# Kernel optimization log

Hardware: AMD Instinct MI355X
Metric: run time of the kernel (lower is better)

The kernel has to match this reference:

```python
import jax, jax.numpy as jnp
import numpy as np

HIDDEN = 128
AUG = 2          # aug_dim
SUBSTEPS = 2     # fixed dopri5 substeps per output interval (replaces adaptive stepping)
B = 16384
T = 8


def _xavier(key, shape, gain=5.0 / 3.0):
    fan_in, fan_out = shape
    lim = gain * np.sqrt(6.0 / (fan_in + fan_out))
    return jax.random.uniform(key, shape, jnp.float32, -lim, lim)


def setup_inputs() -> dict:
    key = jax.random.key(0)
    ks = jax.random.split(key, 4)
    return {
        "r0": jax.random.normal(ks[0], (B, 2), jnp.float32),
        "t": jnp.linspace(0.0, 1.0, T, dtype=jnp.float32),
        "W1": _xavier(ks[1], (5, HIDDEN)),
        "b1": jnp.zeros((HIDDEN,), jnp.float32),
        "W2": _xavier(ks[2], (HIDDEN, HIDDEN)),
        "b2": jnp.zeros((HIDDEN,), jnp.float32),
        "W3": _xavier(ks[3], (HIDDEN, 2)),
        "b3": jnp.zeros((2,), jnp.float32),
    }


def _ode_f(t, s, W1, b1, W2, b2, W3, b3):
    # s: [B, 2+AUG]; t: scalar -> concat time feature, tiny tanh MLP
    tf = t * jnp.ones((s.shape[0], 1), s.dtype)
    inp = jnp.concatenate([s, tf], axis=-1)            # [B, 5]
    h = jnp.tanh(inp @ W1 + b1)                        # [B, 128]
    h = jnp.tanh(h @ W2 + b2)                          # [B, 128]
    v_xy = h @ W3 + b3                                 # [B, 2]
    v_a = jnp.zeros((s.shape[0], AUG), s.dtype)        # static aug dynamics
    return jnp.concatenate([v_xy, v_a], axis=-1)


def _dopri5_step(f, t, s, dt):
    # Dormand-Prince RK45 tableau, 5th-order solution advance (as torchdiffeq dopri5)
    k1 = f(t, s)
    k2 = f(t + dt * (1.0 / 5.0), s + dt * (1.0 / 5.0) * k1)
    k3 = f(t + dt * (3.0 / 10.0), s + dt * ((3.0 / 40.0) * k1 + (9.0 / 40.0) * k2))
    k4 = f(t + dt * (4.0 / 5.0),
           s + dt * ((44.0 / 45.0) * k1 - (56.0 / 15.0) * k2 + (32.0 / 9.0) * k3))
    k5 = f(t + dt * (8.0 / 9.0),
           s + dt * ((19372.0 / 6561.0) * k1 - (25360.0 / 2187.0) * k2
                     + (64448.0 / 6561.0) * k3 - (212.0 / 729.0) * k4))
    k6 = f(t + dt,
           s + dt * ((9017.0 / 3168.0) * k1 - (355.0 / 33.0) * k2
                     + (46732.0 / 5247.0) * k3 + (49.0 / 176.0) * k4
                     - (5103.0 / 18656.0) * k5))
    return s + dt * ((35.0 / 384.0) * k1 + (500.0 / 1113.0) * k3
                     + (125.0 / 192.0) * k4 - (2187.0 / 6784.0) * k5
                     + (11.0 / 84.0) * k6)


def _integrate(r0, t, W1, b1, W2, b2, W3, b3):
    s0 = jnp.concatenate([r0, jnp.zeros((r0.shape[0], AUG), r0.dtype)], axis=-1)
    f = lambda tt, ss: _ode_f(tt, ss, W1, b1, W2, b2, W3, b3)

    def interval(s, ts):
        t0, t1 = ts
        dt = (t1 - t0) / SUBSTEPS
        for j in range(SUBSTEPS):  # small fixed loop, unrolled
            s = _dopri5_step(f, t0 + j * dt, s, dt)
        return s, s

    _, ys = jax.lax.scan(interval, s0, (t[:-1], t[1:]))   # [T-1, B, 4]
    traj = jnp.concatenate([s0[None], ys], axis=0)        # [T, B, 4]
    return jnp.transpose(traj, (1, 0, 2))[..., :2]        # [B, T, 2]


def reference(r0, t, W1, b1, W2, b2, W3, b3):
    return _integrate(r0, t, W1, b1, W2, b2, W3, b3)
```

## Files before the change

### kernel.cpp

```cpp
#include <hip/hip_runtime.h>


#define HID 128
#define TT  8
#define F(a,b) ((float)((double)(a)/(double)(b)))
#define K2C 2.8853900817779268f

typedef __attribute__((ext_vector_type(8))) short bf16x8;
typedef __attribute__((ext_vector_type(4))) float f32x4;
typedef __attribute__((ext_vector_type(2))) float f32x2;

union Frag { bf16x8 v; unsigned short u[8]; unsigned int d[4]; };

__device__ __forceinline__ f32x2 bc(float s) { return f32x2{s, s}; }
__device__ __forceinline__ f32x2 pk_fma(f32x2 a, f32x2 b, f32x2 c) {
#if __has_builtin(__builtin_elementwise_fma)
  return __builtin_elementwise_fma(a, b, c);
#else
  return a * b + c;
#endif
}
__device__ __forceinline__ float exp2_fast(float x) {
#if __has_builtin(__builtin_amdgcn_exp2f)
  return __builtin_amdgcn_exp2f(x);
#else
  return __builtin_exp2f(x);
#endif
}
__device__ __forceinline__ unsigned short f2bf(float f) {
  unsigned u = __builtin_bit_cast(unsigned, f);
  u += 0x7FFFu + ((u >> 16) & 1u);
  return (unsigned short)(u >> 16);
}
__device__ __forceinline__ unsigned pack2bf(float a, float b) {
#if __has_builtin(__builtin_amdgcn_cvt_pk_bf16_f32)
  auto pk = __builtin_amdgcn_cvt_pk_bf16_f32(a, b);
  return __builtin_bit_cast(unsigned, pk);
#else
  unsigned ua = __builtin_bit_cast(unsigned, a);
  unsigned ub = __builtin_bit_cast(unsigned, b);
  ua += 0x7FFFu + ((ua >> 16) & 1u);
  ub += 0x7FFFu + ((ub >> 16) & 1u);
  return __builtin_amdgcn_perm(ub, ua, 0x07060302u);
#endif
}
__device__ __forceinline__ f32x2 sig_q(f32x2 u) {
  f32x2 e;
  e.x = exp2_fast(u.x);
  e.y = exp2_fast(u.y);
  f32x2 d = e + bc(1.0f);
  f32x2 q;
  q.x = __builtin_amdgcn_rcpf(d.x);
  q.y = __builtin_amdgcn_rcpf(d.y);
  return q;
}
__device__ __forceinline__ f32x2 tanh_pre(f32x2 u) {
  return pk_fma(bc(-2.0f), sig_q(u), bc(1.0f));
}

__global__ __launch_bounds__(64, 1) void node_kernel(
    const float* __restrict__ r0, const float* __restrict__ tarr,
    const float* __restrict__ W1, const float* __restrict__ b1,
    const float* __restrict__ W2, const float* __restrict__ b2,
    const float* __restrict__ W3, const float* __restrict__ b3,
    float* __restrict__ out)
{
  const int lane = (int)(threadIdx.x & 63u);
  const int quad = lane >> 4;
  const int m16  = lane & 15;
  const int s    = (int)blockIdx.x * 16 + m16;

  f32x2 w1x[16], w1y[16], w1t[16], bb1[16];
  #pragma unroll
  for (int kk = 0; kk < 4; ++kk)
    #pragma unroll
    for (int p = 0; p < 4; ++p) {
      int i = kk * 32 + quad * 8 + 2 * p;
      int idx = kk * 4 + p;
      w1x[idx] = f32x2{W1[0 * HID + i], W1[0 * HID + i + 1]} * bc(K2C);
      w1y[idx] = f32x2{W1[1 * HID + i], W1[1 * HID + i + 1]} * bc(K2C);
      w1t[idx] = f32x2{W1[4 * HID + i], W1[4 * HID + i + 1]} * bc(K2C);
      bb1[idx] = f32x2{b1[i], b1[i + 1]} * bc(K2C);
    }
  Frag W2f[8][4];
  #pragma unroll
  for (int t = 0; t < 8; ++t) {
    int o = t * 16 + m16;
    #pragma unroll
    for (int kk = 0; kk < 4; ++kk) {
      #pragma unroll
      for (int j = 0; j < 8; ++j)
        W2f[t][kk].u[j] = f2bf(W2[(kk * 32 + quad * 8 + j) * HID + o] * K2C);
      asm volatile("" : "+a"(W2f[t][kk].v));
    }
  }
  f32x4 b2i[8];
  f32x2 w3n2[8][4];
  f32x2 w3s = bc(0.f);
  #pragma unroll
  for (int t = 0; t < 8; ++t) {
    #pragma unroll
    for (int rr = 0; rr < 4; ++rr) {
      int o = t * 16 + quad * 4 + rr;
      b2i[t][rr] = b2[o] * K2C;
      f32x2 w3 = f32x2{W3[o * 2 + 0], W3[o * 2 + 1]};
      w3s += w3;
      w3n2[t][rr] = w3 * bc(-2.f);
    }
    asm volatile("" : "+a"(b2i[t]));
  }
  const f32x2 b3v = f32x2{b3[0], b3[1]};

  f32x2 S = f32x2{r0[2 * s + 0], r0[2 * s + 1]};
  if (lane < 16) *(float2*)&out[(s * TT + 0) * 2] = make_float2(S.x, S.y);

  auto feval = [&](float tt, f32x2 st) -> f32x2 {
    const f32x2 sx = bc(st.x), sy = bc(st.y), tv = bc(tt);
    f32x4 acc[8];
    #pragma unroll
    for (int kk = 0; kk < 4; ++kk) {
      unsigned pd[4];
      #pragma unroll
      for (int p = 0; p < 4; ++p) {
        int idx = kk * 4 + p;
        f32x2 a = pk_fma(sx, w1x[idx], bb1[idx]);
        a = pk_fma(sy, w1y[idx], a);
        a = pk_fma(tv, w1t[idx], a);
        f32x2 h = tanh_pre(a);
        pd[p] = pack2bf(h.x, h.y);
      }
      Frag bv;
      bv.d[0] = pd[0]; bv.d[1] = pd[1]; bv.d[2] = pd[2]; bv.d[3] = pd[3];
      if (kk == 0) {
        #pragma unroll
        for (int t = 0; t < 8; ++t)
          acc[t] = __builtin_amdgcn_mfma_f32_16x16x32_bf16(
              W2f[t][0].v, bv.v, b2i[t], 0, 0, 0);
      } else {
        #pragma unroll
        for (int t = 0; t < 8; ++t)
          acc[t] = __builtin_amdgcn_mfma_f32_16x16x32_bf16(
              W2f[t][kk].v, bv.v, acc[t], 0, 0, 0);
      }
    }
    f32x2 vsa[2] = {w3s, bc(0.f)};
    #pragma unroll
    for (int t = 0; t < 8; ++t)
      #pragma unroll
      for (int p = 0; p < 2; ++p) {
        f32x2 av = f32x2{acc[t][2 * p], acc[t][2 * p + 1]};
        f32x2 q = sig_q(av);
        vsa[t & 1] = pk_fma(bc(q.x), w3n2[t][2 * p + 0], vsa[t & 1]);
        vsa[t & 1] = pk_fma(bc(q.y), w3n2[t][2 * p + 1], vsa[t & 1]);
      }
    f32x2 vs = vsa[0] + vsa[1];
    float px = vs.x, py = vs.y;
    px += __shfl_xor(px, 16); py += __shfl_xor(py, 16);
    px += __shfl_xor(px, 32); py += __shfl_xor(py, 32);
    return f32x2{px, py} + b3v;
  };

  #pragma unroll 1
  for (int iv = 0; iv < TT - 1; ++iv) {
    float t0 = tarr[iv], t1 = tarr[iv + 1];
    float dt = (t1 - t0) * 0.5f;
    #pragma unroll 1
    for (int ss = 0; ss < 2; ++ss) {
      float tb = (ss == 0) ? t0 : (t0 + dt);
      const f32x2 dtv = bc(dt);
      f32x2 k1 = feval(tb, S);
      f32x2 k2 = feval(tb + dt * F(1,5), pk_fma(bc(dt * F(1,5)), k1, S));
      f32x2 a3 = pk_fma(bc(F(9,40)), k2, bc(F(3,40)) * k1);
      f32x2 k3 = feval(tb + dt * F(3,10), pk_fma(dtv, a3, S));
      f32x2 a4 = pk_fma(bc(F(44,45)), k1,
                 pk_fma(bc(-F(56,15)), k2, bc(F(32,9)) * k3));
      f32x2 k4 = feval(tb + dt * F(4,5), pk_fma(dtv, a4, S));
      f32x2 a5 = pk_fma(bc(F(19372,6561)), k1,
                 pk_fma(bc(-F(25360,2187)), k2,
                 pk_fma(bc(F(64448,6561)), k3, bc(-F(212,729)) * k4)));
      f32x2 k5 = feval(tb + dt * F(8,9), pk_fma(dtv, a5, S));
      f32x2 a6 = pk_fma(bc(F(9017,3168)), k1,
                 pk_fma(bc(-F(355,33)), k2,
                 pk_fma(bc(F(46732,5247)), k3,
                 pk_fma(bc(F(49,176)), k4, bc(-F(5103,18656)) * k5))));
      f32x2 k6 = feval(tb + dt, pk_fma(dtv, a6, S));
      f32x2 fin = pk_fma(bc(F(35,384)), k1,
                  pk_fma(bc(F(500,1113)), k3,
                  pk_fma(bc(F(125,192)), k4,
                  pk_fma(bc(-F(2187,6784)), k5, bc(F(11,84)) * k6))));
      S = pk_fma(dtv, fin, S);
    }
    if (lane < 16) *(float2*)&out[(s * TT + iv + 1) * 2] = make_float2(S.x, S.y);
  }
}

extern "C" void kernel_launch(void* const* d_in, const int* in_sizes, int n_in,
                              void* d_out, int out_size, void* d_ws, size_t ws_size,
                              hipStream_t stream) {
  const float* r0 = (const float*)d_in[0];
  const float* t  = (const float*)d_in[1];
  const float* W1 = (const float*)d_in[2];
  const float* b1 = (const float*)d_in[3];
  const float* W2 = (const float*)d_in[4];
  const float* b2 = (const float*)d_in[5];
  const float* W3 = (const float*)d_in[6];
  const float* b3 = (const float*)d_in[7];
  float* out = (float*)d_out;
  const int B = in_sizes[0] / 2;
  dim3 grid(B / 16), block(64);
  node_kernel<<<grid, block, 0, stream>>>(r0, t, W1, b1, W2, b2, W3, b3, out);
}
```

Before: 180.1 us.

## Split each 16-sample MLP evaluation across two wavefronts with LDS exchange

Each block now runs two wavefronts for the same 16 samples. Each wave computes half of the layer-1 hidden units and half of the layer-2 output tiles. Layer-1 bf16 fragments are swapped through shared memory so each wave holds the full input for its MFMAs, and the partial layer-3 sums are combined through shared memory as well. The goal is to halve per-wave register pressure and MFMA/transcendental latency along the serial RK chain, at the cost of two __syncthreads per function evaluation and the LDS traffic that goes with them.

```diff
diff --git a/kernel.cpp b/kernel.cpp
--- a/kernel.cpp
+++ b/kernel.cpp
@@ -58,106 +58,138 @@
   return pk_fma(bc(-2.0f), sig_q(u), bc(1.0f));
 }
 
-__global__ __launch_bounds__(64, 1) void node_kernel(
+__global__ __launch_bounds__(128, 2) void node_kernel(
     const float* __restrict__ r0, const float* __restrict__ tarr,
     const float* __restrict__ W1, const float* __restrict__ b1,
     const float* __restrict__ W2, const float* __restrict__ b2,
     const float* __restrict__ W3, const float* __restrict__ b3,
     float* __restrict__ out)
 {
-  const int lane = (int)(threadIdx.x & 63u);
+  const int tid  = (int)threadIdx.x;
+  const int w    = tid >> 6;
+  const int lane = tid & 63;
   const int quad = lane >> 4;
   const int m16  = lane & 15;
   const int s    = (int)blockIdx.x * 16 + m16;
 
-  f32x2 w1x[16], w1y[16], w1t[16], bb1[16];
+  __shared__ unsigned fragbuf[2][2][64][8];
+  __shared__ float    vredbuf[2][2][16][2];
+
+  f32x2 w1x[8], w1y[8], w1t[8], bb1[8];
   #pragma unroll
-  for (int kk = 0; kk < 4; ++kk)
+  for (int kkl = 0; kkl < 2; ++kkl)
     #pragma unroll
     for (int p = 0; p < 4; ++p) {
-      int i = kk * 32 + quad * 8 + 2 * p;
-      int idx = kk * 4 + p;
+      int i = (2 * w + kkl) * 32 + quad * 8 + 2 * p;
+      int idx = kkl * 4 + p;
       w1x[idx] = f32x2{W1[0 * HID + i], W1[0 * HID + i + 1]} * bc(K2C);
       w1y[idx] = f32x2{W1[1 * HID + i], W1[1 * HID + i + 1]} * bc(K2C);
       w1t[idx] = f32x2{W1[4 * HID + i], W1[4 * HID + i + 1]} * bc(K2C);
       bb1[idx] = f32x2{b1[i], b1[i + 1]} * bc(K2C);
     }
-  Frag W2f[8][4];
+  Frag W2f[4][4];
   #pragma unroll
-  for (int t = 0; t < 8; ++t) {
-    int o = t * 16 + m16;
+  for (int tl = 0; tl < 4; ++tl) {
+    int o = (4 * w + tl) * 16 + m16;
     #pragma unroll
     for (int kk = 0; kk < 4; ++kk) {
       #pragma unroll
       for (int j = 0; j < 8; ++j)
-        W2f[t][kk].u[j] = f2bf(W2[(kk * 32 + quad * 8 + j) * HID + o] * K2C);
-      asm volatile("" : "+a"(W2f[t][kk].v));
+        W2f[tl][kk].u[j] = f2bf(W2[(kk * 32 + quad * 8 + j) * HID + o] * K2C);
+      asm volatile("" : "+a"(W2f[tl][kk].v));
     }
   }
-  f32x4 b2i[8];
-  f32x2 w3n2[8][4];
+  f32x4 b2i[4];
+  f32x2 w3n2[4][4];
   f32x2 w3s = bc(0.f);
   #pragma unroll
-  for (int t = 0; t < 8; ++t) {
+  for (int tl = 0; tl < 4; ++tl) {
     #pragma unroll
     for (int rr = 0; rr < 4; ++rr) {
-      int o = t * 16 + quad * 4 + rr;
-      b2i[t][rr] = b2[o] * K2C;
+      int o = (4 * w + tl) * 16 + quad * 4 + rr;
+      b2i[tl][rr] = b2[o] * K2C;
       f32x2 w3 = f32x2{W3[o * 2 + 0], W3[o * 2 + 1]};
       w3s += w3;
-      w3n2[t][rr] = w3 * bc(-2.f);
-    }
-    asm volatile("" : "+a"(b2i[t]));
+      w3n2[tl][rr] = w3 * bc(-2.f);
+    }
+    asm volatile("" : "+a"(b2i[tl]));
   }
   const f32x2 b3v = f32x2{b3[0], b3[1]};
 
   f32x2 S = f32x2{r0[2 * s + 0], r0[2 * s + 1]};
-  if (lane < 16) *(float2*)&out[(s * TT + 0) * 2] = make_float2(S.x, S.y);
+  if (w == 0 && lane < 16)
+    *(float2*)&out[(s * TT + 0) * 2] = make_float2(S.x, S.y);
+
+  int par = 0;
 
   auto feval = [&](float tt, f32x2 st) -> f32x2 {
     const f32x2 sx = bc(st.x), sy = bc(st.y), tv = bc(tt);
-    f32x4 acc[8];
-    #pragma unroll
-    for (int kk = 0; kk < 4; ++kk) {
+    Frag own0, own1;
+    #pragma unroll
+    for (int kkl = 0; kkl < 2; ++kkl) {
       unsigned pd[4];
       #pragma unroll
       for (int p = 0; p < 4; ++p) {
-        int idx = kk * 4 + p;
+        int idx = kkl * 4 + p;
         f32x2 a = pk_fma(sx, w1x[idx], bb1[idx]);
         a = pk_fma(sy, w1y[idx], a);
         a = pk_fma(tv, w1t[idx], a);
         f32x2 h = tanh_pre(a);
         pd[p] = pack2bf(h.x, h.y);
       }
-      Frag bv;
-      bv.d[0] = pd[0]; bv.d[1] = pd[1]; bv.d[2] = pd[2]; bv.d[3] = pd[3];
-      if (kk == 0) {
-        #pragma unroll
-        for (int t = 0; t < 8; ++t)
-          acc[t] = __builtin_amdgcn_mfma_f32_16x16x32_bf16(
-              W2f[t][0].v, bv.v, b2i[t], 0, 0, 0);
-      } else {
-        #pragma unroll
-        for (int t = 0; t < 8; ++t)
-          acc[t] = __builtin_amdgcn_mfma_f32_16x16x32_bf16(
-              W2f[t][kk].v, bv.v, acc[t], 0, 0, 0);
-      }
-    }
+      Frag& f = kkl ? own1 : own0;
+      f.d[0] = pd[0]; f.d[1] = pd[1]; f.d[2] = pd[2]; f.d[3] = pd[3];
+    }
+    unsigned* dst = &fragbuf[par][w][lane][0];
+    *(uint4*)(dst + 0) = *(uint4*)&own0.d[0];
+    *(uint4*)(dst + 4) = *(uint4*)&own1.d[0];
+    __syncthreads();
+    const unsigned* src = &fragbuf[par][w ^ 1][lane][0];
+    Frag par0, par1;
+    *(uint4*)&par0.d[0] = *(const uint4*)(src + 0);
+    *(uint4*)&par1.d[0] = *(const uint4*)(src + 4);
+    Frag g0, g1, g2, g3;
+    if (w == 0) { g0 = own0; g1 = own1; g2 = par0; g3 = par1; }
+    else        { g0 = par0; g1 = par1; g2 = own0; g3 = own1; }
+    f32x4 acc[4];
+    #pragma unroll
+    for (int tl = 0; tl < 4; ++tl)
+      acc[tl] = __builtin_amdgcn_mfma_f32_16x16x32_bf16(
+          W2f[tl][0].v, g0.v, b2i[tl], 0, 0, 0);
+    #pragma unroll
+    for (int tl = 0; tl < 4; ++tl)
+      acc[tl] = __builtin_amdgcn_mfma_f32_16x16x32_bf16(
+          W2f[tl][1].v, g1.v, acc[tl], 0, 0, 0);
+    #pragma unroll
+    for (int tl = 0; tl < 4; ++tl)
+      acc[tl] = __builtin_amdgcn_mfma_f32_16x16x32_bf16(
+          W2f[tl][2].v, g2.v, acc[tl], 0, 0, 0);
+    #pragma unroll
+    for (int tl = 0; tl < 4; ++tl)
+      acc[tl] = __builtin_amdgcn_mfma_f32_16x16x32_bf16(
+          W2f[tl][3].v, g3.v, acc[tl], 0, 0, 0);
     f32x2 vsa[2] = {w3s, bc(0.f)};
     #pragma unroll
-    for (int t = 0; t < 8; ++t)
+    for (int tl = 0; tl < 4; ++tl)
       #pragma unroll
       for (int p = 0; p < 2; ++p) {
-        f32x2 av = f32x2{acc[t][2 * p], acc[t][2 * p + 1]};
+        f32x2 av = f32x2{acc[tl][2 * p], acc[tl][2 * p + 1]};
         f32x2 q = sig_q(av);
-        vsa[t & 1] = pk_fma(bc(q.x), w3n2[t][2 * p + 0], vsa[t & 1]);
-        vsa[t & 1] = pk_fma(bc(q.y), w3n2[t][2 * p + 1], vsa[t & 1]);
+        vsa[tl & 1] = pk_fma(bc(q.x), w3n2[tl][2 * p + 0], vsa[tl & 1]);
+        vsa[tl & 1] = pk_fma(bc(q.y), w3n2[tl][2 * p + 1], vsa[tl & 1]);
       }
     f32x2 vs = vsa[0] + vsa[1];
     float px = vs.x, py = vs.y;
     px += __shfl_xor(px, 16); py += __shfl_xor(py, 16);
     px += __shfl_xor(px, 32); py += __shfl_xor(py, 32);
-    return f32x2{px, py} + b3v;
+    if (lane < 16) {
+      vredbuf[par][w][m16][0] = px;
+      vredbuf[par][w][m16][1] = py;
+    }
+    __syncthreads();
+    float2 o = *(float2*)&vredbuf[par][w ^ 1][m16][0];
+    par ^= 1;
+    return f32x2{px + o.x, py + o.y} + b3v;
   };
 
   #pragma unroll 1
@@ -190,7 +222,8 @@
                   pk_fma(bc(-F(2187,6784)), k5, bc(F(11,84)) * k6))));
       S = pk_fma(dtv, fin, S);
     }
-    if (lane < 16) *(float2*)&out[(s * TT + iv + 1) * 2] = make_float2(S.x, S.y);
+    if (w == 0 && lane < 16)
+      *(float2*)&out[(s * TT + iv + 1) * 2] = make_float2(S.x, S.y);
   }
 }
 
@@ -207,6 +240,6 @@
   const float* b3 = (const float*)d_in[7];
   float* out = (float*)d_out;
   const int B = in_sizes[0] / 2;
-  dim3 grid(B / 16), block(64);
+  dim3 grid(B / 16), block(128);
   node_kernel<<<grid, block, 0, stream>>>(r0, t, W1, b1, W2, b2, W3, b3, out);
 }
```

Measured after the change: 199.3 us. +10.7%, slower.
